# Kernel tuning notes

Measured on AMD Instinct MI355X. Metric: run time of the kernel, lower is better.

Reference implementation:

```python
import jax, jax.numpy as jnp
import numpy as np

S, A, B, D = 4, 64, 2048, 384
H1, H2, H3 = 128, 128, 64


def setup_inputs() -> dict:
    key = jax.random.key(0)
    ks = jax.random.split(key, 6)
    x = jax.random.normal(ks[0], (B, A, D), dtype=jnp.float32)
    species = jax.random.randint(ks[1], (A,), 0, S, dtype=jnp.int32)
    # per-species stacked MLP weights, scaled ~1/sqrt(fan_in) like reset_parameters
    W0 = jax.random.normal(ks[2], (S, D, H1), dtype=jnp.float32) / np.sqrt(D)
    W1 = jax.random.normal(ks[3], (S, H1, H2), dtype=jnp.float32) / np.sqrt(H1)
    W2 = jax.random.normal(ks[4], (S, H2, H3), dtype=jnp.float32) / np.sqrt(H2)
    W3 = jax.random.normal(ks[5], (S, H3, 1), dtype=jnp.float32) / np.sqrt(H3)
    b0 = jnp.zeros((S, H1), jnp.float32)
    b1 = jnp.zeros((S, H2), jnp.float32)
    b2 = jnp.zeros((S, H3), jnp.float32)
    b3 = jnp.zeros((S, 1), jnp.float32)
    return {"x": x, "species": species, "W0": W0, "b0": b0, "W1": W1,
            "b1": b1, "W2": W2, "b2": b2, "W3": W3, "b3": b3}


def reference(x, species, W0, b0, W1, b1, W2, b2, W3, b3):
    # Gather per-atom species weights once, then batched per-atom GEMMs.
    # x: [B, A, D]; species: [A]
    y = jnp.einsum('bad,adh->bah', x, W0[species]) + b0[species]
    y = jnp.exp(-y * y)
    y = jnp.einsum('bah,ahk->bak', y, W1[species]) + b1[species]
    y = jnp.exp(-y * y)
    y = jnp.einsum('bak,akm->bam', y, W2[species]) + b2[species]
    y = jnp.exp(-y * y)
    y = jnp.einsum('bam,amo->bao', y, W3[species]) + b3[species]  # [B, A, 1]
    return jnp.squeeze(jnp.sum(y, axis=1))  # [B]
```

## Files before the change

### kernel.cpp

```cpp
#include <hip/hip_runtime.h>

#define S_DIM 4
#define A_DIM 64
#define B_DIM 2048
#define D_DIM 384
#define H1D 128
#define H2D 128
#define H3D 64
#define MT 64

typedef __attribute__((ext_vector_type(8))) short short8;
typedef __attribute__((ext_vector_type(4))) float float4v;

__device__ __forceinline__ unsigned short f2bf(float f) {
  unsigned u = __float_as_uint(f);
  u += 0x7FFFu + ((u >> 16) & 1u);
  return (unsigned short)(u >> 16);
}

__device__ __forceinline__ void store_bf4(unsigned short* p, float4v v) {
  union { unsigned short s[4]; uint2 u; } t;
  t.s[0] = f2bf(v[0]); t.s[1] = f2bf(v[1]);
  t.s[2] = f2bf(v[2]); t.s[3] = f2bf(v[3]);
  *(uint2*)p = t.u;
}

__global__ __launch_bounds__(256) void prep_weights(
    const float* __restrict__ W0, const float* __restrict__ W1,
    const float* __restrict__ W2,
    unsigned short* __restrict__ W0T, unsigned short* __restrict__ W1T,
    unsigned short* __restrict__ W2T) {
  __shared__ float tile[32][33];
  int b = blockIdx.x;
  const float* src; unsigned short* dst; int R, C, dt, ht, s;
  if (b < 192) {
    s = b / 48; int t = b % 48; dt = t / 4; ht = t % 4;
    src = W0 + s * D_DIM * H1D; dst = W0T + s * H1D * D_DIM; R = D_DIM; C = H1D;
  } else if (b < 256) {
    int bb = b - 192; s = bb / 16; int t = bb % 16; dt = t / 4; ht = t % 4;
    src = W1 + s * H1D * H2D; dst = W1T + s * H2D * H1D; R = H1D; C = H2D;
  } else {
    int bb = b - 256; s = bb / 8; int t = bb % 8; dt = t / 2; ht = t % 2;
    src = W2 + s * H2D * H3D; dst = W2T + s * H3D * H2D; R = H2D; C = H3D;
  }
  int tx = threadIdx.x & 31, ty = threadIdx.x >> 5;
#pragma unroll
  for (int k = 0; k < 4; ++k)
    tile[ty + 8 * k][tx] = src[(size_t)(dt * 32 + ty + 8 * k) * C + ht * 32 + tx];
  __syncthreads();
#pragma unroll
  for (int k = 0; k < 4; ++k)
    dst[(size_t)(ht * 32 + ty + 8 * k) * R + dt * 32 + tx] = f2bf(tile[tx][ty + 8 * k]);
}

__global__ __launch_bounds__(256, 3) void mlp_fused(
    const float* __restrict__ x, const int* __restrict__ species,
    const unsigned short* __restrict__ W0T, const unsigned short* __restrict__ W1T,
    const unsigned short* __restrict__ W2T,
    const float* __restrict__ b0, const float* __restrict__ b1,
    const float* __restrict__ b2, const float* __restrict__ W3,
    const float* __restrict__ b3, float* __restrict__ out) {
  __shared__ __align__(16) unsigned short bufA[MT * 392];
  __shared__ __align__(16) float W3s[H3D];

  unsigned short* xs = bufA;
  unsigned short* H0 = bufA;
  unsigned short* H1 = bufA + MT * 136;
  float* H2 = (float*)bufA;

  const int a = blockIdx.y;
  const int brow0 = blockIdx.x * MT;
  const int sp = species[a];
  const int tid = threadIdx.x;
  const int wave = tid >> 6;
  const int lane = tid & 63;
  const int q = lane >> 4;
  const int r = lane & 15;

  if (tid < H3D) W3s[tid] = W3[sp * H3D + tid];

  const float4v zero = {0.f, 0.f, 0.f, 0.f};

  const int srow = tid >> 2;
  const int c4 = tid & 3;
  const float* xrow = x + ((size_t)(brow0 + srow) * A_DIM + a) * D_DIM + c4 * 4;
  unsigned short* xdst = xs + srow * 392 + c4 * 4;

  const unsigned short* w0base =
      W0T + (size_t)sp * H1D * D_DIM + (wave * 32 + r) * D_DIM + q * 8;

  float4v xva[8], xvb[8];
#pragma unroll
  for (int j = 0; j < 8; ++j) xva[j] = *(const float4v*)(xrow + j * 16);
#pragma unroll
  for (int j = 0; j < 8; ++j) xvb[j] = *(const float4v*)(xrow + (j + 8) * 16);
  short8 bf0[4][2];
#pragma unroll
  for (int kk = 0; kk < 4; ++kk)
#pragma unroll
    for (int n = 0; n < 2; ++n)
      bf0[kk][n] = *(const short8*)(w0base + n * 16 * D_DIM + kk * 32);
#pragma unroll
  for (int j = 0; j < 8; ++j) store_bf4(xdst + j * 16, xva[j]);
#pragma unroll
  for (int j = 0; j < 8; ++j) xva[j] = *(const float4v*)(xrow + (j + 16) * 16);
#pragma unroll
  for (int j = 0; j < 8; ++j) store_bf4(xdst + (j + 8) * 16, xvb[j]);
#pragma unroll
  for (int j = 0; j < 8; ++j) store_bf4(xdst + (j + 16) * 16, xva[j]);
  __syncthreads();

  float4v acc0[4][2];
#pragma unroll
  for (int g = 0; g < 4; ++g) { acc0[g][0] = zero; acc0[g][1] = zero; }
#pragma unroll
  for (int st = 0; st < 3; ++st) {
    short8 bfs[4][2];
    if (st == 0) {
#pragma unroll
      for (int kk = 0; kk < 4; ++kk) { bfs[kk][0] = bf0[kk][0]; bfs[kk][1] = bf0[kk][1]; }
    } else {
#pragma unroll
      for (int kk = 0; kk < 4; ++kk)
#pragma unroll
        for (int n = 0; n < 2; ++n)
          bfs[kk][n] = *(const short8*)(w0base + n * 16 * D_DIM + st * 128 + kk * 32);
    }
#pragma unroll
    for (int g = 0; g < 4; ++g)
#pragma unroll
      for (int kk = 0; kk < 4; ++kk) {
        short8 af = *(const short8*)(xs + (g * 16 + r) * 392 + st * 128 + kk * 32 + q * 8);
        acc0[g][0] = __builtin_amdgcn_mfma_f32_16x16x32_bf16(af, bfs[kk][0], acc0[g][0], 0, 0, 0);
        acc0[g][1] = __builtin_amdgcn_mfma_f32_16x16x32_bf16(af, bfs[kk][1], acc0[g][1], 0, 0, 0);
      }
  }
  __syncthreads();
  {
    const float* b0p = b0 + sp * H1D;
#pragma unroll
    for (int n = 0; n < 2; ++n) {
      float bias = b0p[wave * 32 + n * 16 + r];
#pragma unroll
      for (int g = 0; g < 4; ++g)
#pragma unroll
        for (int i = 0; i < 4; ++i) {
          float y = acc0[g][n][i] + bias;
          H0[(g * 16 + q * 4 + i) * 136 + wave * 32 + n * 16 + r] = f2bf(__expf(-y * y));
        }
    }
  }
  __syncthreads();

  {
    float4v acc1[4][2];
#pragma unroll
    for (int g = 0; g < 4; ++g) { acc1[g][0] = zero; acc1[g][1] = zero; }
    const unsigned short* w1base =
        W1T + (size_t)sp * H2D * H1D + (wave * 32 + r) * H1D + q * 8;
    short8 bf[4][2];
#pragma unroll
    for (int kk = 0; kk < 4; ++kk)
#pragma unroll
      for (int n = 0; n < 2; ++n)
        bf[kk][n] = *(const short8*)(w1base + n * 16 * H1D + kk * 32);
#pragma unroll
    for (int g = 0; g < 4; ++g)
#pragma unroll
      for (int kk = 0; kk < 4; ++kk) {
        short8 af = *(const short8*)(H0 + (g * 16 + r) * 136 + kk * 32 + q * 8);
        acc1[g][0] = __builtin_amdgcn_mfma_f32_16x16x32_bf16(af, bf[kk][0], acc1[g][0], 0, 0, 0);
        acc1[g][1] = __builtin_amdgcn_mfma_f32_16x16x32_bf16(af, bf[kk][1], acc1[g][1], 0, 0, 0);
      }
    const float* b1p = b1 + sp * H2D;
#pragma unroll
    for (int n = 0; n < 2; ++n) {
      float bias = b1p[wave * 32 + n * 16 + r];
#pragma unroll
      for (int g = 0; g < 4; ++g)
#pragma unroll
        for (int i = 0; i < 4; ++i) {
          float y = acc1[g][n][i] + bias;
          H1[(g * 16 + q * 4 + i) * 136 + wave * 32 + n * 16 + r] = f2bf(__expf(-y * y));
        }
    }
  }
  __syncthreads();

  {
    float4v acc2[4];
#pragma unroll
    for (int g = 0; g < 4; ++g) acc2[g] = zero;
    const unsigned short* w2base =
        W2T + (size_t)sp * H3D * H2D + (wave * 16 + r) * H2D + q * 8;
    short8 bf[4];
#pragma unroll
    for (int kk = 0; kk < 4; ++kk)
      bf[kk] = *(const short8*)(w2base + kk * 32);
#pragma unroll
    for (int g = 0; g < 4; ++g)
#pragma unroll
      for (int kk = 0; kk < 4; ++kk) {
        short8 af = *(const short8*)(H1 + (g * 16 + r) * 136 + kk * 32 + q * 8);
        acc2[g] = __builtin_amdgcn_mfma_f32_16x16x32_bf16(af, bf[kk], acc2[g], 0, 0, 0);
      }
    float bias = b2[sp * H3D + wave * 16 + r];
#pragma unroll
    for (int g = 0; g < 4; ++g)
#pragma unroll
      for (int i = 0; i < 4; ++i) {
        float y = acc2[g][i] + bias;
        H2[(g * 16 + q * 4 + i) * 68 + wave * 16 + r] = __expf(-y * y);
      }
  }
  __syncthreads();

  {
    const int row = tid >> 2;
    const int seg = tid & 3;
    const float4v* h2p = (const float4v*)(H2 + row * 68 + seg * 16);
    const float4v* w3p = (const float4v*)(W3s + seg * 16);
    float4v sv = zero;
#pragma unroll
    for (int jj = 0; jj < 4; ++jj) sv += h2p[jj] * w3p[jj];
    float s = sv[0] + sv[1] + sv[2] + sv[3];
    s += __shfl_xor(s, 1);
    s += __shfl_xor(s, 2);
    if (seg == 0) atomicAdd(&out[brow0 + row], s + b3[sp]);
  }
}

extern "C" void kernel_launch(void* const* d_in, const int* in_sizes, int n_in,
                              void* d_out, int out_size, void* d_ws, size_t ws_size,
                              hipStream_t stream) {
  const float* x       = (const float*)d_in[0];
  const int*   species = (const int*)d_in[1];
  const float* W0 = (const float*)d_in[2];
  const float* b0 = (const float*)d_in[3];
  const float* W1 = (const float*)d_in[4];
  const float* b1 = (const float*)d_in[5];
  const float* W2 = (const float*)d_in[6];
  const float* b2 = (const float*)d_in[7];
  const float* W3 = (const float*)d_in[8];
  const float* b3 = (const float*)d_in[9];
  float* out = (float*)d_out;

  unsigned short* W0T = (unsigned short*)d_ws;
  unsigned short* W1T = W0T + S_DIM * H1D * D_DIM;
  unsigned short* W2T = W1T + S_DIM * H2D * H1D;

  hipMemsetAsync(d_out, 0, out_size * sizeof(float), stream);
  prep_weights<<<dim3(288), dim3(256), 0, stream>>>(W0, W1, W2, W0T, W1T, W2T);
  mlp_fused<<<dim3(B_DIM / MT, A_DIM), dim3(256), 0, stream>>>(
      x, species, W0T, W1T, W2T, b0, b1, b2, W3, b3, out);
}
```

Measured before the change: 318.5 us.

## Load x fragments directly from global into MFMA operands, dropping LDS staging

Layer 0 no longer stages the whole 64x384 x tile in LDS as bf16. Each wave now loads its MFMA A-fragments straight from global memory and converts them to bf16 in registers, so every wave re-reads the same x rows (4x redundant global/L2 traffic). LDS shrinks to two small hidden buffers, which allows occupancy to rise from 3 to 4 blocks per CU. In exchange, the global loads are less coalesced: each lane reads 32B from rows spaced A*D apart. The k-loop is also no longer unrolled.

```diff
diff --git a/kernel.cpp b/kernel.cpp
--- a/kernel.cpp
+++ b/kernel.cpp
@@ -8,6 +8,7 @@
 #define H2D 128
 #define H3D 64
 #define MT 64
+#define XROW (A_DIM * D_DIM)
 
 typedef __attribute__((ext_vector_type(8))) short short8;
 typedef __attribute__((ext_vector_type(4))) float float4v;
@@ -16,13 +17,6 @@
   unsigned u = __float_as_uint(f);
   u += 0x7FFFu + ((u >> 16) & 1u);
   return (unsigned short)(u >> 16);
-}
-
-__device__ __forceinline__ void store_bf4(unsigned short* p, float4v v) {
-  union { unsigned short s[4]; uint2 u; } t;
-  t.s[0] = f2bf(v[0]); t.s[1] = f2bf(v[1]);
-  t.s[2] = f2bf(v[2]); t.s[3] = f2bf(v[3]);
-  *(uint2*)p = t.u;
 }
 
 __global__ __launch_bounds__(256) void prep_weights(
@@ -53,20 +47,17 @@
     dst[(size_t)(ht * 32 + ty + 8 * k) * R + dt * 32 + tx] = f2bf(tile[tx][ty + 8 * k]);
 }
 
-__global__ __launch_bounds__(256, 3) void mlp_fused(
+__global__ __launch_bounds__(256, 4) void mlp_fused(
     const float* __restrict__ x, const int* __restrict__ species,
     const unsigned short* __restrict__ W0T, const unsigned short* __restrict__ W1T,
     const unsigned short* __restrict__ W2T,
     const float* __restrict__ b0, const float* __restrict__ b1,
     const float* __restrict__ b2, const float* __restrict__ W3,
     const float* __restrict__ b3, float* __restrict__ out) {
-  __shared__ __align__(16) unsigned short bufA[MT * 392];
-  __shared__ __align__(16) float W3s[H3D];
-
-  unsigned short* xs = bufA;
-  unsigned short* H0 = bufA;
-  unsigned short* H1 = bufA + MT * 136;
-  float* H2 = (float*)bufA;
+  __shared__ __align__(16) unsigned short H0[MT * 136];
+  __shared__ __align__(16) unsigned short H1[MT * 136];
+  __shared__ float W3s[H3D];
+  float* H2 = (float*)H0;
 
   const int a = blockIdx.y;
   const int brow0 = blockIdx.x * MT;
@@ -81,61 +72,36 @@
 
   const float4v zero = {0.f, 0.f, 0.f, 0.f};
 
-  const int srow = tid >> 2;
-  const int c4 = tid & 3;
-  const float* xrow = x + ((size_t)(brow0 + srow) * A_DIM + a) * D_DIM + c4 * 4;
-  unsigned short* xdst = xs + srow * 392 + c4 * 4;
-
+  float4v acc0[4][2];
+#pragma unroll
+  for (int g = 0; g < 4; ++g) { acc0[g][0] = zero; acc0[g][1] = zero; }
+
+  const float* xb = x + ((size_t)brow0 * A_DIM + a) * D_DIM + (size_t)r * XROW + q * 8;
   const unsigned short* w0base =
       W0T + (size_t)sp * H1D * D_DIM + (wave * 32 + r) * D_DIM + q * 8;
 
-  float4v xva[8], xvb[8];
-#pragma unroll
-  for (int j = 0; j < 8; ++j) xva[j] = *(const float4v*)(xrow + j * 16);
-#pragma unroll
-  for (int j = 0; j < 8; ++j) xvb[j] = *(const float4v*)(xrow + (j + 8) * 16);
-  short8 bf0[4][2];
-#pragma unroll
-  for (int kk = 0; kk < 4; ++kk)
-#pragma unroll
-    for (int n = 0; n < 2; ++n)
-      bf0[kk][n] = *(const short8*)(w0base + n * 16 * D_DIM + kk * 32);
-#pragma unroll
-  for (int j = 0; j < 8; ++j) store_bf4(xdst + j * 16, xva[j]);
-#pragma unroll
-  for (int j = 0; j < 8; ++j) xva[j] = *(const float4v*)(xrow + (j + 16) * 16);
-#pragma unroll
-  for (int j = 0; j < 8; ++j) store_bf4(xdst + (j + 8) * 16, xvb[j]);
-#pragma unroll
-  for (int j = 0; j < 8; ++j) store_bf4(xdst + (j + 16) * 16, xva[j]);
-  __syncthreads();
-
-  float4v acc0[4][2];
-#pragma unroll
-  for (int g = 0; g < 4; ++g) { acc0[g][0] = zero; acc0[g][1] = zero; }
-#pragma unroll
+#pragma unroll 1
   for (int st = 0; st < 3; ++st) {
-    short8 bfs[4][2];
-    if (st == 0) {
-#pragma unroll
-      for (int kk = 0; kk < 4; ++kk) { bfs[kk][0] = bf0[kk][0]; bfs[kk][1] = bf0[kk][1]; }
-    } else {
-#pragma unroll
-      for (int kk = 0; kk < 4; ++kk)
-#pragma unroll
-        for (int n = 0; n < 2; ++n)
-          bfs[kk][n] = *(const short8*)(w0base + n * 16 * D_DIM + st * 128 + kk * 32);
+    const int ks = st * 128;
+#pragma unroll
+    for (int kk = 0; kk < 4; ++kk) {
+      short8 bn0 = *(const short8*)(w0base + ks + kk * 32);
+      short8 bn1 = *(const short8*)(w0base + 16 * D_DIM + ks + kk * 32);
+#pragma unroll
+      for (int g = 0; g < 4; ++g) {
+        const float* ap = xb + (size_t)g * 16 * XROW + ks + kk * 32;
+        float4v a0 = *(const float4v*)ap;
+        float4v a1 = *(const float4v*)(ap + 4);
+        short8 af;
+        af[0] = (short)f2bf(a0[0]); af[1] = (short)f2bf(a0[1]);
+        af[2] = (short)f2bf(a0[2]); af[3] = (short)f2bf(a0[3]);
+        af[4] = (short)f2bf(a1[0]); af[5] = (short)f2bf(a1[1]);
+        af[6] = (short)f2bf(a1[2]); af[7] = (short)f2bf(a1[3]);
+        acc0[g][0] = __builtin_amdgcn_mfma_f32_16x16x32_bf16(af, bn0, acc0[g][0], 0, 0, 0);
+        acc0[g][1] = __builtin_amdgcn_mfma_f32_16x16x32_bf16(af, bn1, acc0[g][1], 0, 0, 0);
+      }
     }
-#pragma unroll
-    for (int g = 0; g < 4; ++g)
-#pragma unroll
-      for (int kk = 0; kk < 4; ++kk) {
-        short8 af = *(const short8*)(xs + (g * 16 + r) * 392 + st * 128 + kk * 32 + q * 8);
-        acc0[g][0] = __builtin_amdgcn_mfma_f32_16x16x32_bf16(af, bfs[kk][0], acc0[g][0], 0, 0, 0);
-        acc0[g][1] = __builtin_amdgcn_mfma_f32_16x16x32_bf16(af, bfs[kk][1], acc0[g][1], 0, 0, 0);
-      }
-  }
-  __syncthreads();
+  }
   {
     const float* b0p = b0 + sp * H1D;
 #pragma unroll
```

Measured after the change: 356.1 us. +11.8%, slower.

## Stream x tiles through double-buffered LDS chunks to overlap loads with MFMA

Applied to the files above, without the earlier changes.

Replaces the single 64x392 bf16 LDS staging of the whole x row with two 64x136 buffers. Each 128-wide K chunk is loaded while the previous chunk's MFMAs run, and later layers reuse the buffers. This shrinks LDS per block and raises the occupancy hint to 4 blocks per CU, aiming to hide HBM latency on this memory-bound x stream. The occupancy hint risks register pressure or spills, and adds barriers between chunks.

```diff
diff --git a/kernel.cpp b/kernel.cpp
--- a/kernel.cpp
+++ b/kernel.cpp
@@ -53,20 +53,19 @@
     dst[(size_t)(ht * 32 + ty + 8 * k) * R + dt * 32 + tx] = f2bf(tile[tx][ty + 8 * k]);
 }
 
-__global__ __launch_bounds__(256, 3) void mlp_fused(
+__global__ __launch_bounds__(256, 4) void mlp_fused(
     const float* __restrict__ x, const int* __restrict__ species,
     const unsigned short* __restrict__ W0T, const unsigned short* __restrict__ W1T,
     const unsigned short* __restrict__ W2T,
     const float* __restrict__ b0, const float* __restrict__ b1,
     const float* __restrict__ b2, const float* __restrict__ W3,
     const float* __restrict__ b3, float* __restrict__ out) {
-  __shared__ __align__(16) unsigned short bufA[MT * 392];
-  __shared__ __align__(16) float W3s[H3D];
-
-  unsigned short* xs = bufA;
-  unsigned short* H0 = bufA;
-  unsigned short* H1 = bufA + MT * 136;
-  float* H2 = (float*)bufA;
+  __shared__ __align__(16) unsigned short xbuf0[MT * 136];
+  __shared__ __align__(16) unsigned short xbuf1[MT * 136];
+  __shared__ float W3s[H3D];
+  unsigned short* H0 = xbuf1;
+  unsigned short* H1 = xbuf0;
+  float* H2 = (float*)xbuf1;
 
   const int a = blockIdx.y;
   const int brow0 = blockIdx.x * MT;
@@ -77,65 +76,87 @@
   const int q = lane >> 4;
   const int r = lane & 15;
 
-  if (tid < H3D) W3s[tid] = W3[sp * H3D + tid];
-
   const float4v zero = {0.f, 0.f, 0.f, 0.f};
 
   const int srow = tid >> 2;
   const int c4 = tid & 3;
   const float* xrow = x + ((size_t)(brow0 + srow) * A_DIM + a) * D_DIM + c4 * 4;
-  unsigned short* xdst = xs + srow * 392 + c4 * 4;
-
   const unsigned short* w0base =
       W0T + (size_t)sp * H1D * D_DIM + (wave * 32 + r) * D_DIM + q * 8;
 
-  float4v xva[8], xvb[8];
-#pragma unroll
-  for (int j = 0; j < 8; ++j) xva[j] = *(const float4v*)(xrow + j * 16);
-#pragma unroll
-  for (int j = 0; j < 8; ++j) xvb[j] = *(const float4v*)(xrow + (j + 8) * 16);
-  short8 bf0[4][2];
+  float4v xv[8];
+#pragma unroll
+  for (int j = 0; j < 8; ++j) xv[j] = *(const float4v*)(xrow + j * 16);
+  if (tid < H3D) W3s[tid] = W3[sp * H3D + tid];
+  short8 bf[4][2];
 #pragma unroll
   for (int kk = 0; kk < 4; ++kk)
 #pragma unroll
     for (int n = 0; n < 2; ++n)
-      bf0[kk][n] = *(const short8*)(w0base + n * 16 * D_DIM + kk * 32);
-#pragma unroll
-  for (int j = 0; j < 8; ++j) store_bf4(xdst + j * 16, xva[j]);
-#pragma unroll
-  for (int j = 0; j < 8; ++j) xva[j] = *(const float4v*)(xrow + (j + 16) * 16);
-#pragma unroll
-  for (int j = 0; j < 8; ++j) store_bf4(xdst + (j + 8) * 16, xvb[j]);
-#pragma unroll
-  for (int j = 0; j < 8; ++j) store_bf4(xdst + (j + 16) * 16, xva[j]);
+      bf[kk][n] = *(const short8*)(w0base + n * 16 * D_DIM + kk * 32);
+  {
+    unsigned short* xd = xbuf0 + srow * 136 + c4 * 4;
+#pragma unroll
+    for (int j = 0; j < 8; ++j) store_bf4(xd + j * 16, xv[j]);
+  }
   __syncthreads();
 
   float4v acc0[4][2];
 #pragma unroll
   for (int g = 0; g < 4; ++g) { acc0[g][0] = zero; acc0[g][1] = zero; }
-#pragma unroll
-  for (int st = 0; st < 3; ++st) {
-    short8 bfs[4][2];
-    if (st == 0) {
-#pragma unroll
-      for (int kk = 0; kk < 4; ++kk) { bfs[kk][0] = bf0[kk][0]; bfs[kk][1] = bf0[kk][1]; }
-    } else {
-#pragma unroll
-      for (int kk = 0; kk < 4; ++kk)
-#pragma unroll
-        for (int n = 0; n < 2; ++n)
-          bfs[kk][n] = *(const short8*)(w0base + n * 16 * D_DIM + st * 128 + kk * 32);
-    }
-#pragma unroll
-    for (int g = 0; g < 4; ++g)
-#pragma unroll
-      for (int kk = 0; kk < 4; ++kk) {
-        short8 af = *(const short8*)(xs + (g * 16 + r) * 392 + st * 128 + kk * 32 + q * 8);
-        acc0[g][0] = __builtin_amdgcn_mfma_f32_16x16x32_bf16(af, bfs[kk][0], acc0[g][0], 0, 0, 0);
-        acc0[g][1] = __builtin_amdgcn_mfma_f32_16x16x32_bf16(af, bfs[kk][1], acc0[g][1], 0, 0, 0);
-      }
-  }
-  __syncthreads();
+
+#pragma unroll
+  for (int j = 0; j < 8; ++j) xv[j] = *(const float4v*)(xrow + 128 + j * 16);
+#pragma unroll
+  for (int g = 0; g < 4; ++g)
+#pragma unroll
+    for (int kk = 0; kk < 4; ++kk) {
+      short8 af = *(const short8*)(xbuf0 + (g * 16 + r) * 136 + kk * 32 + q * 8);
+      acc0[g][0] = __builtin_amdgcn_mfma_f32_16x16x32_bf16(af, bf[kk][0], acc0[g][0], 0, 0, 0);
+      acc0[g][1] = __builtin_amdgcn_mfma_f32_16x16x32_bf16(af, bf[kk][1], acc0[g][1], 0, 0, 0);
+    }
+  {
+    unsigned short* xd = xbuf1 + srow * 136 + c4 * 4;
+#pragma unroll
+    for (int j = 0; j < 8; ++j) store_bf4(xd + j * 16, xv[j]);
+  }
+  __syncthreads();
+
+#pragma unroll
+  for (int kk = 0; kk < 4; ++kk)
+#pragma unroll
+    for (int n = 0; n < 2; ++n)
+      bf[kk][n] = *(const short8*)(w0base + n * 16 * D_DIM + 128 + kk * 32);
+#pragma unroll
+  for (int j = 0; j < 8; ++j) xv[j] = *(const float4v*)(xrow + 256 + j * 16);
+#pragma unroll
+  for (int g = 0; g < 4; ++g)
+#pragma unroll
+    for (int kk = 0; kk < 4; ++kk) {
+      short8 af = *(const short8*)(xbuf1 + (g * 16 + r) * 136 + kk * 32 + q * 8);
+      acc0[g][0] = __builtin_amdgcn_mfma_f32_16x16x32_bf16(af, bf[kk][0], acc0[g][0], 0, 0, 0);
+      acc0[g][1] = __builtin_amdgcn_mfma_f32_16x16x32_bf16(af, bf[kk][1], acc0[g][1], 0, 0, 0);
+    }
+  {
+    unsigned short* xd = xbuf0 + srow * 136 + c4 * 4;
+#pragma unroll
+    for (int j = 0; j < 8; ++j) store_bf4(xd + j * 16, xv[j]);
+  }
+  __syncthreads();
+
+#pragma unroll
+  for (int kk = 0; kk < 4; ++kk)
+#pragma unroll
+    for (int n = 0; n < 2; ++n)
+      bf[kk][n] = *(const short8*)(w0base + n * 16 * D_DIM + 256 + kk * 32);
+#pragma unroll
+  for (int g = 0; g < 4; ++g)
+#pragma unroll
+    for (int kk = 0; kk < 4; ++kk) {
+      short8 af = *(const short8*)(xbuf0 + (g * 16 + r) * 136 + kk * 32 + q * 8);
+      acc0[g][0] = __builtin_amdgcn_mfma_f32_16x16x32_bf16(af, bf[kk][0], acc0[g][0], 0, 0, 0);
+      acc0[g][1] = __builtin_amdgcn_mfma_f32_16x16x32_bf16(af, bf[kk][1], acc0[g][1], 0, 0, 0);
+    }
   {
     const float* b0p = b0 + sp * H1D;
 #pragma unroll
@@ -158,19 +179,19 @@
     for (int g = 0; g < 4; ++g) { acc1[g][0] = zero; acc1[g][1] = zero; }
     const unsigned short* w1base =
         W1T + (size_t)sp * H2D * H1D + (wave * 32 + r) * H1D + q * 8;
-    short8 bf[4][2];
+    short8 wf[4][2];
 #pragma unroll
     for (int kk = 0; kk < 4; ++kk)
 #pragma unroll
       for (int n = 0; n < 2; ++n)
-        bf[kk][n] = *(const short8*)(w1base + n * 16 * H1D + kk * 32);
+        wf[kk][n] = *(const short8*)(w1base + n * 16 * H1D + kk * 32);
 #pragma unroll
     for (int g = 0; g < 4; ++g)
 #pragma unroll
       for (int kk = 0; kk < 4; ++kk) {
         short8 af = *(const short8*)(H0 + (g * 16 + r) * 136 + kk * 32 + q * 8);
-        acc1[g][0] = __builtin_amdgcn_mfma_f32_16x16x32_bf16(af, bf[kk][0], acc1[g][0], 0, 0, 0);
-        acc1[g][1] = __builtin_amdgcn_mfma_f32_16x16x32_bf16(af, bf[kk][1], acc1[g][1], 0, 0, 0);
+        acc1[g][0] = __builtin_amdgcn_mfma_f32_16x16x32_bf16(af, wf[kk][0], acc1[g][0], 0, 0, 0);
+        acc1[g][1] = __builtin_amdgcn_mfma_f32_16x16x32_bf16(af, wf[kk][1], acc1[g][1], 0, 0, 0);
       }
     const float* b1p = b1 + sp * H2D;
 #pragma unroll
@@ -193,16 +214,16 @@
     for (int g = 0; g < 4; ++g) acc2[g] = zero;
     const unsigned short* w2base =
         W2T + (size_t)sp * H3D * H2D + (wave * 16 + r) * H2D + q * 8;
-    short8 bf[4];
+    short8 wf[4];
 #pragma unroll
     for (int kk = 0; kk < 4; ++kk)
-      bf[kk] = *(const short8*)(w2base + kk * 32);
+      wf[kk] = *(const short8*)(w2base + kk * 32);
 #pragma unroll
     for (int g = 0; g < 4; ++g)
 #pragma unroll
       for (int kk = 0; kk < 4; ++kk) {
         short8 af = *(const short8*)(H1 + (g * 16 + r) * 136 + kk * 32 + q * 8);
-        acc2[g] = __builtin_amdgcn_mfma_f32_16x16x32_bf16(af, bf[kk], acc2[g], 0, 0, 0);
+        acc2[g] = __builtin_amdgcn_mfma_f32_16x16x32_bf16(af, wf[kk], acc2[g], 0, 0, 0);
       }
     float bias = b2[sp * H3D + wave * 16 + r];
 #pragma unroll
```

Result: faster. 310.3 us (-2.6%).
